# Optimization experiments

Measured on AMD Instinct MI355X. Metric: run time of the kernel, lower is better.

The kernel has to match this reference:

```python
import jax, jax.numpy as jnp
import numpy as np
from jax import lax


def _layernorm(x, g, b, eps=1e-5):
    mu = x.mean(-1, keepdims=True)
    var = ((x - mu) ** 2).mean(-1, keepdims=True)
    return (x - mu) * lax.rsqrt(var + eps) * g + b


def _conv1d(x, w, b):
    # x: (B, T, Cin), w: (K, Cin, Cout) -> (B, T, Cout), SAME padding
    return lax.conv_general_dilated(x, w, (1,), 'SAME',
                                    dimension_numbers=('NWC', 'WIO', 'NWC')) + b


def _gated(x, wf, bf, wg, bg):
    return jax.nn.relu(_conv1d(x, wf, bf)) * jax.nn.sigmoid(_conv1d(x, wg, bg))


def setup_inputs() -> dict:
    key = jax.random.key(0)
    ks = iter(jax.random.split(key, 32))
    B, T, F, H = 32, 1024, 64, 768
    ch = H // 3
    d = {'x': jax.random.normal(next(ks), (B, T, F), jnp.float32)}
    for k in (3, 5, 7):
        d[f'conv{k}_wf'] = jax.random.normal(next(ks), (k, F, ch), jnp.float32) * 0.05
        d[f'conv{k}_bf'] = jnp.zeros((ch,), jnp.float32)
        d[f'conv{k}_wg'] = jax.random.normal(next(ks), (k, F, ch), jnp.float32) * 0.05
        d[f'conv{k}_bg'] = jnp.zeros((ch,), jnp.float32)
    d['conv_ln_g'] = jnp.ones((H,), jnp.float32)
    d['conv_ln_b'] = jnp.zeros((H,), jnp.float32)
    for name in ('gqa_wq', 'gqa_wk', 'gqa_wv', 'gqa_wp'):
        d[name] = jax.random.normal(next(ks), (2, H, H), jnp.float32) * 0.02
    d['gqa_bp'] = jnp.zeros((2, H), jnp.float32)
    d['gqa_ln_g'] = jnp.ones((2, H), jnp.float32)
    d['gqa_ln_b'] = jnp.zeros((2, H), jnp.float32)
    d['proj_w'] = jax.random.normal(next(ks), (2 * H, H), jnp.float32) * 0.02
    d['proj_b'] = jnp.zeros((H,), jnp.float32)
    d['proj_ln_g'] = jnp.ones((H,), jnp.float32)
    d['proj_ln_b'] = jnp.zeros((H,), jnp.float32)
    return d


def _gqa(h, wq, wk, wv, wp, bp, ln_g, ln_b, n_groups=4):
    B, T, H = h.shape
    G, D = n_groups, H // n_groups
    scale = D ** -0.5
    Q = (h @ wq).reshape(B, T, G, D)
    K = (h @ wk).reshape(B, T, G, D)
    V = (h @ wv).reshape(B, T, G, D)
    attn = jax.nn.softmax(jnp.einsum('bqgd,bkgd->bgqk', Q, K) * scale, axis=-1)
    out = jnp.einsum('bgqk,bkgd->bqgd', attn, V).reshape(B, T, H)
    return _layernorm(h + out @ wp + bp, ln_g, ln_b)


def reference(x, conv3_wf, conv3_bf, conv3_wg, conv3_bg,
              conv5_wf, conv5_bf, conv5_wg, conv5_bg,
              conv7_wf, conv7_bf, conv7_wg, conv7_bg,
              conv_ln_g, conv_ln_b,
              gqa_wq, gqa_wk, gqa_wv, gqa_wp, gqa_bp, gqa_ln_g, gqa_ln_b,
              proj_w, proj_b, proj_ln_g, proj_ln_b):
    # Multi-scale gated conv front end (SAME padding -> all branches length T)
    o3 = _gated(x, conv3_wf, conv3_bf, conv3_wg, conv3_bg)
    o5 = _gated(x, conv5_wf, conv5_bf, conv5_wg, conv5_bg)
    o7 = _gated(x, conv7_wf, conv7_bf, conv7_wg, conv7_bg)
    h = _layernorm(jnp.concatenate([o3, o5, o7], axis=-1), conv_ln_g, conv_ln_b)
    # Two GQA blocks
    for i in range(2):
        h = _gqa(h, gqa_wq[i], gqa_wk[i], gqa_wv[i], gqa_wp[i],
                 gqa_bp[i], gqa_ln_g[i], gqa_ln_b[i])
    # mean + population-std pooling over time
    m = h.mean(axis=1)
    s = jnp.sqrt(((h - m[:, None, :]) ** 2).mean(axis=1))
    z = jnp.concatenate([m, s], axis=-1) @ proj_w + proj_b
    return jax.nn.relu(_layernorm(z, proj_ln_g, proj_ln_b))
```

## Files before the change

### kernel.cpp

```cpp
#include <hip/hip_runtime.h>
#include <hip/hip_bf16.h>


constexpr int Bb = 32, Tt = 1024, Ff = 64, Hh = 768, Gg = 4, Dd = 192;
constexpr float EPS = 1e-5f;
constexpr int WKMAX = 448;
constexpr int VTS = 40;

typedef __attribute__((ext_vector_type(8))) short short8;
typedef __attribute__((ext_vector_type(4))) float floatx4;

__device__ __forceinline__ void async_copy16(const void* g, void* l) {
  __builtin_amdgcn_global_load_lds(
      (const __attribute__((address_space(1))) unsigned int*)g,
      (__attribute__((address_space(3))) unsigned int*)l, 16, 0, 0);
}

__device__ __forceinline__ short bf16s(float f) {
  __hip_bfloat16 h = __float2bfloat16(f);
  return *(short*)&h;
}

__device__ __forceinline__ unsigned int pack_bf16(float lo, float hi) {
  return (unsigned int)(unsigned short)bf16s(lo) |
         ((unsigned int)(unsigned short)bf16s(hi) << 16);
}

__device__ __forceinline__ float2 block_reduce2(float a, float b, float* tmp) {
  int lane = threadIdx.x & 63, wid = threadIdx.x >> 6;
#pragma unroll
  for (int off = 32; off > 0; off >>= 1) {
    a += __shfl_down(a, off);
    b += __shfl_down(b, off);
  }
  if (lane == 0) { tmp[wid] = a; tmp[4 + wid] = b; }
  __syncthreads();
  if (threadIdx.x == 0) {
    tmp[0] = tmp[0] + tmp[1] + tmp[2] + tmp[3];
    tmp[4] = tmp[4] + tmp[5] + tmp[6] + tmp[7];
  }
  __syncthreads();
  float2 r; r.x = tmp[0]; r.y = tmp[4];
  return r;
}

__global__ __launch_bounds__(256) void wt_cast_kernel(
    const float* __restrict__ wq, const float* __restrict__ wk,
    const float* __restrict__ wv, const float* __restrict__ wp,
    __hip_bfloat16* __restrict__ wt) {
  const int z = blockIdx.z;
  const int m = z & 3, i = z >> 2;
  const float* src =
      (m == 0 ? wq : m == 1 ? wk : m == 2 ? wv : wp) + (size_t)i * Hh * Hh;
  const float sc = (m == 0) ? 0.0721687836f : 1.f;
  __shared__ float tile[32][33];
  const int n0 = blockIdx.x * 32, k0 = blockIdx.y * 32;
  const int tx = threadIdx.x & 31, ty = threadIdx.x >> 5;
#pragma unroll
  for (int r = 0; r < 4; r++)
    tile[ty + 8 * r][tx] = src[(size_t)(k0 + ty + 8 * r) * Hh + n0 + tx];
  __syncthreads();
#pragma unroll
  for (int r = 0; r < 4; r++)
    wt[((size_t)z * Hh + n0 + ty + 8 * r) * Hh + k0 + tx] =
        __float2bfloat16(tile[tx][ty + 8 * r] * sc);
}

__global__ __launch_bounds__(256) void wcv_cast_kernel(
    const float* __restrict__ wf3, const float* __restrict__ wg3,
    const float* __restrict__ wf5, const float* __restrict__ wg5,
    const float* __restrict__ wf7, const float* __restrict__ wg7,
    __hip_bfloat16* __restrict__ wcv) {
  int idx = blockIdx.x * 256 + threadIdx.x;
  if (idx >= 3 * 512 * WKMAX) return;
  int j = idx / (512 * WKMAX);
  int rem = idx - j * 512 * WKMAX;
  int n = rem / WKMAX, k = rem % WKMAX;
  int Kw = 3 + 2 * j;
  float v = 0.f;
  if (k < Kw * 64) {
    const float* src = (n < 256) ? (j == 0 ? wf3 : j == 1 ? wf5 : wf7)
                                 : (j == 0 ? wg3 : j == 1 ? wg5 : wg7);
    v = src[(size_t)k * 256 + (n & 255)];
  }
  wcv[idx] = __float2bfloat16(v);
}

__global__ __launch_bounds__(256) void x_cast_kernel(
    const float* __restrict__ x, short* __restrict__ x16, int n8) {
  int idx = blockIdx.x * 256 + threadIdx.x;
  if (idx >= n8) return;
  const float4 a = ((const float4*)x)[idx * 2];
  const float4 b = ((const float4*)x)[idx * 2 + 1];
  short8 o;
  o[0] = bf16s(a.x); o[1] = bf16s(a.y); o[2] = bf16s(a.z); o[3] = bf16s(a.w);
  o[4] = bf16s(b.x); o[5] = bf16s(b.y); o[6] = bf16s(b.z); o[7] = bf16s(b.w);
  ((short8*)x16)[idx] = o;
}

__global__ __launch_bounds__(256) void conv_gemm_kernel(
    const short* __restrict__ x16, const short* __restrict__ wcv,
    short* __restrict__ yraw, int b0) {
  __shared__ __align__(16) short Asl[128 * 72];
  __shared__ __align__(16) short Bsl[128 * 72];
  const int t0 = blockIdx.x * 128, n0 = blockIdx.y * 128;
  const int bl = blockIdx.z / 3, j = blockIdx.z % 3;
  const int Kw = 3 + 2 * j, pad = j + 1;
  const int bglob = b0 + bl;
  const short* wb = wcv + (size_t)j * 512 * WKMAX;
  const int tid = threadIdx.x;
  const int lane = tid & 63;
  const int w = tid >> 6, wm = w >> 1, wn = w & 1;
  const int lm = lane & 15, quad = lane >> 4;

  floatx4 acc[4][4];
#pragma unroll
  for (int i = 0; i < 4; i++)
#pragma unroll
    for (int jj = 0; jj < 4; jj++) acc[i][jj] = (floatx4)0.f;

  for (int kk = 0; kk < Kw; kk++) {
    __syncthreads();
#pragma unroll
    for (int it = 0; it < 4; it++) {
      int s = it * 256 + tid;
      int row = s >> 3, c8 = s & 7;
      int t = t0 + row + kk - pad;
      short8 av = (short8)0;
      if (t >= 0 && t < Tt)
        av = *(const short8*)&x16[((size_t)bglob * Tt + t) * Ff + c8 * 8];
      *(short8*)&Asl[row * 72 + c8 * 8] = av;
      short8 bv = *(const short8*)&wb[(size_t)(n0 + row) * WKMAX + kk * 64 +
                                      c8 * 8];
      *(short8*)&Bsl[row * 72 + c8 * 8] = bv;
    }
    __syncthreads();
#pragma unroll
    for (int ks = 0; ks < 2; ks++) {
      short8 a[4], b[4];
#pragma unroll
      for (int i = 0; i < 4; i++)
        a[i] = *(const short8*)&Asl[(wm * 64 + i * 16 + lm) * 72 + ks * 32 +
                                    quad * 8];
#pragma unroll
      for (int jj = 0; jj < 4; jj++)
        b[jj] = *(const short8*)&Bsl[(wn * 64 + jj * 16 + lm) * 72 + ks * 32 +
                                     quad * 8];
#pragma unroll
      for (int i = 0; i < 4; i++)
#pragma unroll
        for (int jj = 0; jj < 4; jj++)
          acc[i][jj] = __builtin_amdgcn_mfma_f32_16x16x32_bf16(a[i], b[jj],
                                                               acc[i][jj],
                                                               0, 0, 0);
    }
  }

  const int rbase = quad * 4;
#pragma unroll
  for (int i = 0; i < 4; i++)
#pragma unroll
    for (int jj = 0; jj < 4; jj++) {
      int mrow = t0 + wm * 64 + i * 16 + rbase;
      int ncol = n0 + wn * 64 + jj * 16 + lm;
#pragma unroll
      for (int r = 0; r < 4; r++)
        yraw[((size_t)bl * Tt + mrow + r) * 1536 + j * 512 + ncol] =
            bf16s(acc[i][jj][r]);
    }
}

__global__ __launch_bounds__(256) void gate_ln_kernel(
    const short* __restrict__ yraw, __hip_bfloat16* __restrict__ h16,
    const float* __restrict__ bf3, const float* __restrict__ bg3,
    const float* __restrict__ bf5, const float* __restrict__ bg5,
    const float* __restrict__ bf7, const float* __restrict__ bg7,
    const float* __restrict__ g, const float* __restrict__ bt) {
  __shared__ float red[8];
  const size_t row = blockIdx.x;
  float v[3], s = 0.f, ss = 0.f;
#pragma unroll
  for (int jj = 0; jj < 3; jj++) {
    int c = threadIdx.x + jj * 256;
    int br = c >> 8, cc = c & 255;
    const float* bfp = br == 0 ? bf3 : br == 1 ? bf5 : bf7;
    const float* bgp = br == 0 ? bg3 : br == 1 ? bg5 : bg7;
    __hip_bfloat16 rf = *(const __hip_bfloat16*)&yraw[row * 1536 + br * 512 + cc];
    __hip_bfloat16 rg =
        *(const __hip_bfloat16*)&yraw[row * 1536 + br * 512 + 256 + cc];
    float f = __bfloat162float(rf) + bfp[cc];
    float gt = __bfloat162float(rg) + bgp[cc];
    float a = f > 0.f ? f : 0.f;
    float t = a * (1.f / (1.f + __expf(-gt)));
    v[jj] = t; s += t; ss += t * t;
  }
  float2 r = block_reduce2(s, ss, red);
  float mu = r.x * (1.f / Hh);
  float var = r.y * (1.f / Hh) - mu * mu;
  float rs = rsqrtf(var + EPS);
#pragma unroll
  for (int jj = 0; jj < 3; jj++) {
    int c = threadIdx.x + jj * 256;
    float o = (v[jj] - mu) * rs * g[c] + bt[c];
    h16[row * Hh + c] = __float2bfloat16(o);
  }
}

__global__ __launch_bounds__(256) void res_ln_kernel(
    __hip_bfloat16* __restrict__ h16, const __hip_bfloat16* __restrict__ y,
    const float* __restrict__ bp, const float* __restrict__ g,
    const float* __restrict__ bt) {
  __shared__ float red[8];
  const size_t row = blockIdx.x;
  float v[3], s = 0.f, ss = 0.f;
#pragma unroll
  for (int jj = 0; jj < 3; jj++) {
    int c = threadIdx.x + jj * 256;
    float t = __bfloat162float(h16[row * Hh + c]) +
              __bfloat162float(y[row * Hh + c]) + bp[c];
    v[jj] = t; s += t; ss += t * t;
  }
  float2 r = block_reduce2(s, ss, red);
  float mu = r.x * (1.f / Hh);
  float var = r.y * (1.f / Hh) - mu * mu;
  float rs = rsqrtf(var + EPS);
#pragma unroll
  for (int jj = 0; jj < 3; jj++) {
    int c = threadIdx.x + jj * 256;
    float o = (v[jj] - mu) * rs * g[c] + bt[c];
    h16[row * Hh + c] = __float2bfloat16(o);
  }
}

__global__ __launch_bounds__(256) void gemm_qkv(
    const short* __restrict__ A, const short* __restrict__ Bt,
    short* __restrict__ q16, short* __restrict__ k16,
    short* __restrict__ vt16) {
  constexpr int K = 768;
  __shared__ __align__(16) short Asl[128 * 32];
  __shared__ __align__(16) short Bsl[128 * 32];
  const int n0 = blockIdx.x * 128, m0 = blockIdx.y * 128;
  const int lane = threadIdx.x & 63;
  const int w = threadIdx.x >> 6, wm = w >> 1, wn = w & 1;
  const int lm = lane & 15, quad = lane >> 4;

  floatx4 acc[4][4];
#pragma unroll
  for (int i = 0; i < 4; i++)
#pragma unroll
    for (int jj = 0; jj < 4; jj++) acc[i][jj] = (floatx4)0.f;

  for (int k0 = 0; k0 < K; k0 += 32) {
    __syncthreads();
#pragma unroll
    for (int half = 0; half < 2; half++) {
      int s = half * 256 + threadIdx.x;
      int m = s >> 2, ks = (s & 3) * 8;
      async_copy16(&A[(size_t)(m0 + m) * K + k0 + ks], &Asl[s * 8]);
      async_copy16(&Bt[(size_t)(n0 + m) * K + k0 + ks], &Bsl[s * 8]);
    }
    __syncthreads();

    short8 a[4], b[4];
#pragma unroll
    for (int i = 0; i < 4; i++)
      a[i] = *(const short8*)&Asl[(wm * 64 + i * 16 + lm) * 32 + quad * 8];
#pragma unroll
    for (int jj = 0; jj < 4; jj++)
      b[jj] = *(const short8*)&Bsl[(wn * 64 + jj * 16 + lm) * 32 + quad * 8];
#pragma unroll
    for (int i = 0; i < 4; i++)
#pragma unroll
      for (int jj = 0; jj < 4; jj++)
        acc[i][jj] = __builtin_amdgcn_mfma_f32_16x16x32_bf16(a[i], b[jj],
                                                             acc[i][jj],
                                                             0, 0, 0);
  }

  const int which = blockIdx.x / 6;
  const int rbase = quad * 4;
#pragma unroll
  for (int i = 0; i < 4; i++)
#pragma unroll
    for (int jj = 0; jj < 4; jj++) {
      int mrow = m0 + wm * 64 + i * 16 + rbase;
      int nl = n0 - which * Hh + wn * 64 + jj * 16 + lm;
      if (which == 0) {
#pragma unroll
        for (int r = 0; r < 4; r++)
          q16[(size_t)(mrow + r) * Hh + nl] = bf16s(acc[i][jj][r]);
      } else if (which == 1) {
#pragma unroll
        for (int r = 0; r < 4; r++)
          k16[(size_t)(mrow + r) * Hh + nl] = bf16s(acc[i][jj][r]);
      } else {
        int bL = mrow >> 10, t = mrow & 1023;
        int g = nl / Dd, d = nl % Dd;
        short4 sv;
        sv.x = bf16s(acc[i][jj][0]); sv.y = bf16s(acc[i][jj][1]);
        sv.z = bf16s(acc[i][jj][2]); sv.w = bf16s(acc[i][jj][3]);
        *(short4*)&vt16[(((size_t)bL * Gg + g) * Dd + d) * Tt + t] = sv;
      }
    }
}

__global__ __launch_bounds__(256) void gemm_proj(
    const short* __restrict__ A, const short* __restrict__ Bt,
    short* __restrict__ C) {
  constexpr int K = 768, N = 768;
  __shared__ __align__(16) short Asl[128 * 32];
  __shared__ __align__(16) short Bsl[128 * 32];
  const int n0 = blockIdx.x * 128, m0 = blockIdx.y * 128;
  const int lane = threadIdx.x & 63;
  const int w = threadIdx.x >> 6, wm = w >> 1, wn = w & 1;
  const int lm = lane & 15, quad = lane >> 4;

  floatx4 acc[4][4];
#pragma unroll
  for (int i = 0; i < 4; i++)
#pragma unroll
    for (int jj = 0; jj < 4; jj++) acc[i][jj] = (floatx4)0.f;

  for (int k0 = 0; k0 < K; k0 += 32) {
    __syncthreads();
#pragma unroll
    for (int half = 0; half < 2; half++) {
      int s = half * 256 + threadIdx.x;
      int m = s >> 2, ks = (s & 3) * 8;
      async_copy16(&A[(size_t)(m0 + m) * K + k0 + ks], &Asl[s * 8]);
      async_copy16(&Bt[(size_t)(n0 + m) * K + k0 + ks], &Bsl[s * 8]);
    }
    __syncthreads();

    short8 a[4], b[4];
#pragma unroll
    for (int i = 0; i < 4; i++)
      a[i] = *(const short8*)&Asl[(wm * 64 + i * 16 + lm) * 32 + quad * 8];
#pragma unroll
    for (int jj = 0; jj < 4; jj++)
      b[jj] = *(const short8*)&Bsl[(wn * 64 + jj * 16 + lm) * 32 + quad * 8];
#pragma unroll
    for (int i = 0; i < 4; i++)
#pragma unroll
      for (int jj = 0; jj < 4; jj++)
        acc[i][jj] = __builtin_amdgcn_mfma_f32_16x16x32_bf16(a[i], b[jj],
                                                             acc[i][jj],
                                                             0, 0, 0);
  }

  const int rbase = quad * 4;
#pragma unroll
  for (int i = 0; i < 4; i++)
#pragma unroll
    for (int jj = 0; jj < 4; jj++) {
      int mrow = m0 + wm * 64 + i * 16 + rbase;
      int ncol = n0 + wn * 64 + jj * 16 + lm;
#pragma unroll
      for (int r = 0; r < 4; r++)
        C[(size_t)(mrow + r) * N + ncol] = bf16s(acc[i][jj][r]);
    }
}

__global__ __launch_bounds__(256, 2) void attn_mfma(
    const short* __restrict__ q16, const short* __restrict__ k16,
    const short* __restrict__ vt16, short* __restrict__ o16) {
  const int b = blockIdx.x;
  const int g = blockIdx.y;
  const int q0 = blockIdx.z * 128;
  const int tid = threadIdx.x;
  const int w = tid >> 6, lane = tid & 63, lm = lane & 15, quad = lane >> 4;

  __shared__ __align__(16) short Ks[32 * 200];
  __shared__ __align__(16) short Vt[192 * VTS];

  short8 qf[2][6];
#pragma unroll
  for (int mt = 0; mt < 2; mt++)
#pragma unroll
    for (int ks = 0; ks < 6; ks++) {
      int tok = b * Tt + q0 + w * 32 + mt * 16 + lm;
      qf[mt][ks] = *(const short8*)&q16[(size_t)tok * Hh + g * Dd + ks * 32 +
                                        quad * 8];
    }

  floatx4 Oa[2][12];
#pragma unroll
  for (int mt = 0; mt < 2; mt++)
#pragma unroll
    for (int n = 0; n < 12; n++) Oa[mt][n] = (floatx4)0.f;
  float mr[2] = {-1e30f, -1e30f}, lr[2] = {0.f, 0.f};

  short8 kvK[3], kvV[3];
#pragma unroll
  for (int it = 0; it < 3; it++) {
    int s = it * 256 + tid;
    int row = s / 24, cs = s - row * 24;
    kvK[it] = *(const short8*)&k16[(size_t)(b * Tt + row) * Hh + g * Dd +
                                   cs * 8];
    int d = s >> 2, c2 = s & 3;
    kvV[it] = *(const short8*)&vt16[(((size_t)b * Gg + g) * Dd + d) * Tt +
                                    c2 * 8];
  }

  for (int kt = 0; kt < Tt; kt += 32) {
    __syncthreads();
#pragma unroll
    for (int it = 0; it < 3; it++) {
      int s = it * 256 + tid;
      int row = s / 24, cs = s - row * 24;
      *(short8*)&Ks[row * 200 + cs * 8] = kvK[it];
      int d = s >> 2, c2 = s & 3;
      *(short8*)&Vt[d * VTS + c2 * 8] = kvV[it];
    }
    __syncthreads();

    if (kt + 32 < Tt) {
#pragma unroll
      for (int it = 0; it < 3; it++) {
        int s = it * 256 + tid;
        int row = s / 24, cs = s - row * 24;
        kvK[it] = *(const short8*)&k16[(size_t)(b * Tt + kt + 32 + row) * Hh +
                                       g * Dd + cs * 8];
        int d = s >> 2, c2 = s & 3;
        kvV[it] = *(const short8*)&vt16[(((size_t)b * Gg + g) * Dd + d) * Tt +
                                        kt + 32 + c2 * 8];
      }
    }

    floatx4 st[2][2];
#pragma unroll
    for (int mt = 0; mt < 2; mt++)
#pragma unroll
      for (int jj = 0; jj < 2; jj++) st[mt][jj] = (floatx4)0.f;
#pragma unroll
    for (int ks = 0; ks < 6; ks++) {
      short8 k0 = *(const short8*)&Ks[lm * 200 + ks * 32 + quad * 8];
      short8 k1 = *(const short8*)&Ks[(16 + lm) * 200 + ks * 32 + quad * 8];
      st[0][0] = __builtin_amdgcn_mfma_f32_16x16x32_bf16(k0, qf[0][ks], st[0][0], 0, 0, 0);
      st[0][1] = __builtin_amdgcn_mfma_f32_16x16x32_bf16(k1, qf[0][ks], st[0][1], 0, 0, 0);
      st[1][0] = __builtin_amdgcn_mfma_f32_16x16x32_bf16(k0, qf[1][ks], st[1][0], 0, 0, 0);
      st[1][1] = __builtin_amdgcn_mfma_f32_16x16x32_bf16(k1, qf[1][ks], st[1][1], 0, 0, 0);
    }

    short8 ptf[2];
#pragma unroll
    for (int mt = 0; mt < 2; mt++) {
      float smax = st[mt][0][0];
#pragma unroll
      for (int r = 1; r < 4; r++) smax = fmaxf(smax, st[mt][0][r]);
#pragma unroll
      for (int r = 0; r < 4; r++) smax = fmaxf(smax, st[mt][1][r]);
      smax = fmaxf(smax, __shfl_xor(smax, 16));
      smax = fmaxf(smax, __shfl_xor(smax, 32));
      float mnew = fmaxf(mr[mt], smax);
      float alpha = __expf(mr[mt] - mnew);
      mr[mt] = mnew;
      float p[2][4];
      float sum = 0.f;
#pragma unroll
      for (int jj = 0; jj < 2; jj++)
#pragma unroll
        for (int r = 0; r < 4; r++) {
          p[jj][r] = __expf(st[mt][jj][r] - mnew);
          sum += p[jj][r];
        }
      sum += __shfl_xor(sum, 16);
      sum += __shfl_xor(sum, 32);
      lr[mt] = lr[mt] * alpha + sum;

      int pk00 = (int)pack_bf16(p[0][0], p[0][1]);
      int pk01 = (int)pack_bf16(p[0][2], p[0][3]);
      int pk10 = (int)pack_bf16(p[1][0], p[1][1]);
      int pk11 = (int)pack_bf16(p[1][2], p[1][3]);
      int srcA = ((quad & 1) << 5) + lm;
      int srcB = srcA + 16;
      int a0 = __shfl(pk00, srcA), a1 = __shfl(pk01, srcA);
      int a2 = __shfl(pk00, srcB), a3 = __shfl(pk01, srcB);
      int b0 = __shfl(pk10, srcA), b1 = __shfl(pk11, srcA);
      int b2 = __shfl(pk10, srcB), b3 = __shfl(pk11, srcB);
      bool hi = quad >= 2;
      union { int u[4]; short8 v; } pu;
      pu.u[0] = hi ? b0 : a0;
      pu.u[1] = hi ? b1 : a1;
      pu.u[2] = hi ? b2 : a2;
      pu.u[3] = hi ? b3 : a3;
      ptf[mt] = pu.v;

#pragma unroll
      for (int n = 0; n < 12; n++)
#pragma unroll
        for (int r = 0; r < 4; r++) Oa[mt][n][r] *= alpha;
    }

#pragma unroll
    for (int n = 0; n < 12; n++) {
      short8 vf = *(const short8*)&Vt[(n * 16 + lm) * VTS + quad * 8];
      Oa[0][n] = __builtin_amdgcn_mfma_f32_16x16x32_bf16(vf, ptf[0], Oa[0][n], 0, 0, 0);
      Oa[1][n] = __builtin_amdgcn_mfma_f32_16x16x32_bf16(vf, ptf[1], Oa[1][n], 0, 0, 0);
    }
  }

#pragma unroll
  for (int mt = 0; mt < 2; mt++) {
    float inv = 1.f / lr[mt];
    int tok = b * Tt + q0 + w * 32 + mt * 16 + lm;
#pragma unroll
    for (int n = 0; n < 12; n++) {
      short4 sv;
      sv.x = bf16s(Oa[mt][n][0] * inv);
      sv.y = bf16s(Oa[mt][n][1] * inv);
      sv.z = bf16s(Oa[mt][n][2] * inv);
      sv.w = bf16s(Oa[mt][n][3] * inv);
      *(short4*)&o16[(size_t)tok * Hh + g * Dd + n * 16 + quad * 4] = sv;
    }
  }
}

__global__ __launch_bounds__(256) void pool_stage1(
    const __hip_bfloat16* __restrict__ h16, float* __restrict__ ppart,
    int b0) {
  int idx = blockIdx.x * 256 + threadIdx.x;
  int seg = blockIdx.y;
  int bl = idx / Hh, c = idx % Hh;
  float s = 0.f, ss = 0.f;
  const __hip_bfloat16* hp = &h16[((size_t)bl * Tt + seg * 128) * Hh + c];
  for (int t = 0; t < 128; t++) {
    float v = __bfloat162float(hp[(size_t)t * Hh]);
    s += v; ss += v * v;
  }
  float* o = &ppart[(((size_t)(b0 + bl) * 8 + seg) * 2) * Hh + c];
  o[0] = s;
  o[Hh] = ss;
}

__global__ __launch_bounds__(256) void pool_stage2(
    const float* __restrict__ ppart, float* __restrict__ pool) {
  int idx = blockIdx.x * 256 + threadIdx.x;
  int b = idx / Hh, c = idx % Hh;
  float s = 0.f, ss = 0.f;
#pragma unroll
  for (int seg = 0; seg < 8; seg++) {
    const float* o = &ppart[(((size_t)b * 8 + seg) * 2) * Hh + c];
    s += o[0]; ss += o[Hh];
  }
  float mu = s * (1.f / Tt);
  float var = ss * (1.f / Tt) - mu * mu;
  pool[(size_t)b * 1536 + c] = mu;
  pool[(size_t)b * 1536 + 768 + c] = sqrtf(fmaxf(var, 0.f));
}

__global__ __launch_bounds__(256) void final_partial(
    const float* __restrict__ pool, const float* __restrict__ pw,
    float* __restrict__ part) {
  const int n = blockIdx.x * 256 + threadIdx.x;
  const int bg = blockIdx.y * 4;
  const int ks = blockIdx.z, k0 = ks * 192;
  __shared__ float ms[4][192];
  for (int e = threadIdx.x; e < 4 * 192; e += 256) {
    int bb = e / 192, kk = e % 192;
    ms[bb][kk] = pool[(size_t)(bg + bb) * 1536 + k0 + kk];
  }
  __syncthreads();
  float a0 = 0.f, a1 = 0.f, a2 = 0.f, a3 = 0.f;
  for (int kk = 0; kk < 192; kk++) {
    float wv = pw[(size_t)(k0 + kk) * Hh + n];
    a0 = fmaf(ms[0][kk], wv, a0);
    a1 = fmaf(ms[1][kk], wv, a1);
    a2 = fmaf(ms[2][kk], wv, a2);
    a3 = fmaf(ms[3][kk], wv, a3);
  }
  part[((size_t)ks * Bb + bg + 0) * Hh + n] = a0;
  part[((size_t)ks * Bb + bg + 1) * Hh + n] = a1;
  part[((size_t)ks * Bb + bg + 2) * Hh + n] = a2;
  part[((size_t)ks * Bb + bg + 3) * Hh + n] = a3;
}

__global__ __launch_bounds__(256) void final_stage2(
    const float* __restrict__ part, const float* __restrict__ pb,
    const float* __restrict__ g, const float* __restrict__ bt,
    float* __restrict__ out) {
  __shared__ float red[8];
  const int b = blockIdx.x;
  float v[3], s = 0.f, ss = 0.f;
#pragma unroll
  for (int jj = 0; jj < 3; jj++) {
    int n = threadIdx.x + jj * 256;
    float a = pb[n];
#pragma unroll
    for (int ks = 0; ks < 8; ks++) a += part[((size_t)ks * Bb + b) * Hh + n];
    v[jj] = a; s += a; ss += a * a;
  }
  float2 r = block_reduce2(s, ss, red);
  float mu = r.x * (1.f / Hh);
  float var = r.y * (1.f / Hh) - mu * mu;
  float rs = rsqrtf(var + EPS);
#pragma unroll
  for (int jj = 0; jj < 3; jj++) {
    int n = threadIdx.x + jj * 256;
    float o = (v[jj] - mu) * rs * g[n] + bt[n];
    out[(size_t)b * Hh + n] = o > 0.f ? o : 0.f;
  }
}

extern "C" void kernel_launch(void* const* d_in, const int* in_sizes, int n_in,
                              void* d_out, int out_size, void* d_ws,
                              size_t ws_size, hipStream_t stream) {
  (void)in_sizes; (void)n_in; (void)out_size;
  const float* x = (const float*)d_in[0];
  const float* cw[3][4];
  for (int j = 0; j < 3; j++)
    for (int p2 = 0; p2 < 4; p2++) cw[j][p2] = (const float*)d_in[1 + j * 4 + p2];
  const float* conv_ln_g = (const float*)d_in[13];
  const float* conv_ln_b = (const float*)d_in[14];
  const float* wq = (const float*)d_in[15];
  const float* wk = (const float*)d_in[16];
  const float* wv = (const float*)d_in[17];
  const float* wp = (const float*)d_in[18];
  const float* bp = (const float*)d_in[19];
  const float* lng = (const float*)d_in[20];
  const float* lnb = (const float*)d_in[21];
  const float* proj_w = (const float*)d_in[22];
  const float* proj_b = (const float*)d_in[23];
  const float* proj_ln_g = (const float*)d_in[24];
  const float* proj_ln_b = (const float*)d_in[25];
  float* out = (float*)d_out;

  const size_t perb = (size_t)Tt * Hh;
  const size_t fixedB = 8ull * Hh * Hh * 2 + 3ull * 512 * WKMAX * 2 +
                        (size_t)Bb * Tt * Ff * 2 + (size_t)Bb * 2 * Hh * 4 +
                        (size_t)Bb * 8 * 2 * Hh * 4 + 8ull * Bb * Hh * 4;
  int chunk = Bb;
  while (chunk > 1 && 8ull * perb * chunk + fixedB > ws_size) chunk >>= 1;

  const size_t crow = perb * (size_t)chunk;
  char* p = (char*)d_ws;
  __hip_bfloat16* h16 = (__hip_bfloat16*)p;  p += crow * 2;
  short* q16 = (short*)p;            p += crow * 2;
  short* k16 = (short*)p;            p += crow * 2;
  short* v16t = (short*)p;           p += crow * 2;
  short* yraw16 = q16;
  short* y16 = k16;
  __hip_bfloat16* wt = (__hip_bfloat16*)p;   p += 8ull * Hh * Hh * 2;
  __hip_bfloat16* wcv = (__hip_bfloat16*)p;  p += 3ull * 512 * WKMAX * 2;
  short* x16 = (short*)p;            p += (size_t)Bb * Tt * Ff * 2;
  float* pool = (float*)p;           p += (size_t)Bb * 2 * Hh * 4;
  float* ppart = (float*)p;          p += (size_t)Bb * 8 * 2 * Hh * 4;
  float* fpart = (float*)p;

  wt_cast_kernel<<<dim3(24, 24, 8), 256, 0, stream>>>(wq, wk, wv, wp, wt);
  wcv_cast_kernel<<<(3 * 512 * WKMAX + 255) / 256, 256, 0, stream>>>(
      cw[0][0], cw[0][2], cw[1][0], cw[1][2], cw[2][0], cw[2][2], wcv);
  x_cast_kernel<<<(Bb * Tt * Ff / 8 + 255) / 256, 256, 0, stream>>>(
      x, x16, Bb * Tt * Ff / 8);

  const short* wts = (const short*)wt;

  for (int b0 = 0; b0 < Bb; b0 += chunk) {
    const int M = chunk * Tt;

    conv_gemm_kernel<<<dim3(Tt / 128, 4, chunk * 3), 256, 0, stream>>>(
        x16, (const short*)wcv, yraw16, b0);
    gate_ln_kernel<<<M, 256, 0, stream>>>(
        yraw16, h16, cw[0][1], cw[0][3], cw[1][1], cw[1][3], cw[2][1],
        cw[2][3], conv_ln_g, conv_ln_b);

    for (int i = 0; i < 2; i++) {
      const short* wqkv = wts + (size_t)(i * 4) * Hh * Hh;
      const short* wtp = wts + (size_t)(i * 4 + 3) * Hh * Hh;
      gemm_qkv<<<dim3(18, M / 128), 256, 0, stream>>>((const short*)h16, wqkv,
                                                      q16, k16, v16t);
      attn_mfma<<<dim3(chunk, Gg, Tt / 128), 256, 0, stream>>>(q16, k16, v16t,
                                                               q16);
      gemm_proj<<<dim3(6, M / 128), 256, 0, stream>>>(q16, wtp, y16);
      res_ln_kernel<<<M, 256, 0, stream>>>(h16, (const __hip_bfloat16*)y16,
                                           bp + (size_t)i * Hh,
                                           lng + (size_t)i * Hh,
                                           lnb + (size_t)i * Hh);
    }

    pool_stage1<<<dim3((chunk * Hh) / 256, 8), 256, 0, stream>>>(h16, ppart,
                                                                 b0);
  }

  pool_stage2<<<(Bb * Hh) / 256, 256, 0, stream>>>(ppart, pool);
  final_partial<<<dim3(3, 8, 8), 256, 0, stream>>>(pool, proj_w, fpart);
  final_stage2<<<Bb, 256, 0, stream>>>(fpart, proj_b, proj_ln_g, proj_ln_b,
                                       out);
}
```

Measured before the change: 1.066 ms.

## Double-buffer K/V tiles in attention and fold row-sum into MFMA

The attention kernel now keeps two LDS buffers for K and V^T tiles, cutting the per-iteration barrier count from two to one and prefetching two tiles ahead in registers. It also appends a ones-row to the V^T tile so a 13th MFMA column accumulates the softmax denominator, replacing the per-tile shuffle reductions for the row sum. The cost is roughly double the LDS footprint, which may reduce occupancy, one extra MFMA per tile, and a denominator summed from bf16-rounded probabilities.

```diff
diff --git a/kernel.cpp b/kernel.cpp
--- a/kernel.cpp
+++ b/kernel.cpp
@@ -370,8 +370,16 @@
   const int tid = threadIdx.x;
   const int w = tid >> 6, lane = tid & 63, lm = lane & 15, quad = lane >> 4;
 
-  __shared__ __align__(16) short Ks[32 * 200];
-  __shared__ __align__(16) short Vt[192 * VTS];
+  __shared__ __align__(16) short Ks[2][32 * 200];
+  __shared__ __align__(16) short Vt[2][208 * VTS];
+
+  for (int e = tid; e < 2 * 16 * VTS; e += 256) {
+    int buf = e / (16 * VTS);
+    int r = e - buf * (16 * VTS);
+    int row = r / VTS, c = r - row * VTS;
+    Vt[buf][(192 + row) * VTS + c] =
+        (row == 0 && c < 32) ? (short)0x3F80 : (short)0;
+  }
 
   short8 qf[2][6];
 #pragma unroll
@@ -383,49 +391,62 @@
                                         quad * 8];
     }
 
-  floatx4 Oa[2][12];
+  floatx4 Oa[2][13];
 #pragma unroll
   for (int mt = 0; mt < 2; mt++)
 #pragma unroll
-    for (int n = 0; n < 12; n++) Oa[mt][n] = (floatx4)0.f;
-  float mr[2] = {-1e30f, -1e30f}, lr[2] = {0.f, 0.f};
-
-  short8 kvK[3], kvV[3];
+    for (int n = 0; n < 13; n++) Oa[mt][n] = (floatx4)0.f;
+  float mr[2] = {-1e30f, -1e30f};
+
+  int krow[3], kcs[3], vrow[3], vcs[3];
+  const short* kgp[3];
+  const short* vgp[3];
 #pragma unroll
   for (int it = 0; it < 3; it++) {
     int s = it * 256 + tid;
-    int row = s / 24, cs = s - row * 24;
-    kvK[it] = *(const short8*)&k16[(size_t)(b * Tt + row) * Hh + g * Dd +
-                                   cs * 8];
-    int d = s >> 2, c2 = s & 3;
-    kvV[it] = *(const short8*)&vt16[(((size_t)b * Gg + g) * Dd + d) * Tt +
-                                    c2 * 8];
-  }
-
-  for (int kt = 0; kt < Tt; kt += 32) {
-    __syncthreads();
-#pragma unroll
-    for (int it = 0; it < 3; it++) {
-      int s = it * 256 + tid;
-      int row = s / 24, cs = s - row * 24;
-      *(short8*)&Ks[row * 200 + cs * 8] = kvK[it];
-      int d = s >> 2, c2 = s & 3;
-      *(short8*)&Vt[d * VTS + c2 * 8] = kvV[it];
-    }
-    __syncthreads();
-
-    if (kt + 32 < Tt) {
+    krow[it] = s / 24; kcs[it] = s - krow[it] * 24;
+    vrow[it] = s >> 2; vcs[it] = s & 3;
+    kgp[it] = &k16[(size_t)(b * Tt + krow[it]) * Hh + g * Dd + kcs[it] * 8];
+    vgp[it] = &vt16[(((size_t)b * Gg + g) * Dd + vrow[it]) * Tt + vcs[it] * 8];
+  }
+
+  short8 kvK[3], kvV[3];
+#pragma unroll
+  for (int it = 0; it < 3; it++) {
+    kvK[it] = *(const short8*)kgp[it];
+    kvV[it] = *(const short8*)vgp[it];
+  }
+#pragma unroll
+  for (int it = 0; it < 3; it++) {
+    *(short8*)&Ks[0][krow[it] * 200 + kcs[it] * 8] = kvK[it];
+    *(short8*)&Vt[0][vrow[it] * VTS + vcs[it] * 8] = kvV[it];
+  }
+#pragma unroll
+  for (int it = 0; it < 3; it++) {
+    kvK[it] = *(const short8*)(kgp[it] + (size_t)32 * Hh);
+    kvV[it] = *(const short8*)(vgp[it] + 32);
+  }
+  __syncthreads();
+
+  for (int i = 0; i < 32; i++) {
+    const int ib = i & 1;
+    if (i + 1 < 32) {
+      const int wb2 = ib ^ 1;
 #pragma unroll
       for (int it = 0; it < 3; it++) {
-        int s = it * 256 + tid;
-        int row = s / 24, cs = s - row * 24;
-        kvK[it] = *(const short8*)&k16[(size_t)(b * Tt + kt + 32 + row) * Hh +
-                                       g * Dd + cs * 8];
-        int d = s >> 2, c2 = s & 3;
-        kvV[it] = *(const short8*)&vt16[(((size_t)b * Gg + g) * Dd + d) * Tt +
-                                        kt + 32 + c2 * 8];
+        *(short8*)&Ks[wb2][krow[it] * 200 + kcs[it] * 8] = kvK[it];
+        *(short8*)&Vt[wb2][vrow[it] * VTS + vcs[it] * 8] = kvV[it];
       }
     }
+    if (i + 2 < 32) {
+      const size_t ko = (size_t)(i + 2) * 32 * Hh;
+      const int vo = (i + 2) * 32;
+#pragma unroll
+      for (int it = 0; it < 3; it++) {
+        kvK[it] = *(const short8*)(kgp[it] + ko);
+        kvV[it] = *(const short8*)(vgp[it] + vo);
+      }
+    }
 
     floatx4 st[2][2];
 #pragma unroll
@@ -434,8 +455,8 @@
       for (int jj = 0; jj < 2; jj++) st[mt][jj] = (floatx4)0.f;
 #pragma unroll
     for (int ks = 0; ks < 6; ks++) {
-      short8 k0 = *(const short8*)&Ks[lm * 200 + ks * 32 + quad * 8];
-      short8 k1 = *(const short8*)&Ks[(16 + lm) * 200 + ks * 32 + quad * 8];
+      short8 k0 = *(const short8*)&Ks[ib][lm * 200 + ks * 32 + quad * 8];
+      short8 k1 = *(const short8*)&Ks[ib][(16 + lm) * 200 + ks * 32 + quad * 8];
       st[0][0] = __builtin_amdgcn_mfma_f32_16x16x32_bf16(k0, qf[0][ks], st[0][0], 0, 0, 0);
       st[0][1] = __builtin_amdgcn_mfma_f32_16x16x32_bf16(k1, qf[0][ks], st[0][1], 0, 0, 0);
       st[1][0] = __builtin_amdgcn_mfma_f32_16x16x32_bf16(k0, qf[1][ks], st[1][0], 0, 0, 0);
@@ -456,17 +477,10 @@
       float alpha = __expf(mr[mt] - mnew);
       mr[mt] = mnew;
       float p[2][4];
-      float sum = 0.f;
 #pragma unroll
       for (int jj = 0; jj < 2; jj++)
 #pragma unroll
-        for (int r = 0; r < 4; r++) {
-          p[jj][r] = __expf(st[mt][jj][r] - mnew);
-          sum += p[jj][r];
-        }
-      sum += __shfl_xor(sum, 16);
-      sum += __shfl_xor(sum, 32);
-      lr[mt] = lr[mt] * alpha + sum;
+        for (int r = 0; r < 4; r++) p[jj][r] = __expf(st[mt][jj][r] - mnew);
 
       int pk00 = (int)pack_bf16(p[0][0], p[0][1]);
       int pk01 = (int)pack_bf16(p[0][2], p[0][3]);
@@ -487,22 +501,24 @@
       ptf[mt] = pu.v;
 
 #pragma unroll
-      for (int n = 0; n < 12; n++)
+      for (int n = 0; n < 13; n++)
 #pragma unroll
         for (int r = 0; r < 4; r++) Oa[mt][n][r] *= alpha;
     }
 
 #pragma unroll
-    for (int n = 0; n < 12; n++) {
-      short8 vf = *(const short8*)&Vt[(n * 16 + lm) * VTS + quad * 8];
+    for (int n = 0; n < 13; n++) {
+      short8 vf = *(const short8*)&Vt[ib][(n * 16 + lm) * VTS + quad * 8];
       Oa[0][n] = __builtin_amdgcn_mfma_f32_16x16x32_bf16(vf, ptf[0], Oa[0][n], 0, 0, 0);
       Oa[1][n] = __builtin_amdgcn_mfma_f32_16x16x32_bf16(vf, ptf[1], Oa[1][n], 0, 0, 0);
     }
+    __syncthreads();
   }
 
 #pragma unroll
   for (int mt = 0; mt < 2; mt++) {
-    float inv = 1.f / lr[mt];
+    float lval = __shfl(Oa[mt][12][0], lm);
+    float inv = 1.f / lval;
     int tok = b * Tt + q0 + w * 32 + mt * 16 + lm;
 #pragma unroll
     for (int n = 0; n < 12; n++) {
```

Result: no change. 1.048 ms (-1.7%).

## Restructure attention: 64-query blocks, async double-buffered V, MFMA row-sum

Applied to the files above, without the earlier changes.

The attention kernel now gives each wave 16 query rows instead of 32, halving accumulator registers so occupancy can rise to 4 blocks per CU. The grid is flattened with batch-group varying fastest so neighbouring blocks share K/V. V tiles are loaded with global_load_lds async copies into a double buffer, and K is still staged through registers. The softmax denominator is computed by a 13th MFMA against a ones-padded V row rather than shuffle reductions; this adds MFMA work and LDS use, and QK work per block is amortised over fewer queries.

```diff
diff --git a/kernel.cpp b/kernel.cpp
--- a/kernel.cpp
+++ b/kernel.cpp
@@ -5,7 +5,6 @@
 constexpr int Bb = 32, Tt = 1024, Ff = 64, Hh = 768, Gg = 4, Dd = 192;
 constexpr float EPS = 1e-5f;
 constexpr int WKMAX = 448;
-constexpr int VTS = 40;
 
 typedef __attribute__((ext_vector_type(8))) short short8;
 typedef __attribute__((ext_vector_type(4))) float floatx4;
@@ -361,158 +360,145 @@
     }
 }
 
-__global__ __launch_bounds__(256, 2) void attn_mfma(
+__global__ __launch_bounds__(256, 4) void attn_mfma(
     const short* __restrict__ q16, const short* __restrict__ k16,
-    const short* __restrict__ vt16, short* __restrict__ o16) {
-  const int b = blockIdx.x;
-  const int g = blockIdx.y;
-  const int q0 = blockIdx.z * 128;
+    const short* __restrict__ vt16, short* __restrict__ o16, int chunk4) {
+  const int bg = blockIdx.x % chunk4;
+  const int qb = blockIdx.x / chunk4;
+  const int b = bg >> 2, g = bg & 3;
+  const int q0 = qb * 64;
   const int tid = threadIdx.x;
   const int w = tid >> 6, lane = tid & 63, lm = lane & 15, quad = lane >> 4;
 
   __shared__ __align__(16) short Ks[32 * 200];
-  __shared__ __align__(16) short Vt[192 * VTS];
-
-  short8 qf[2][6];
-#pragma unroll
-  for (int mt = 0; mt < 2; mt++)
-#pragma unroll
-    for (int ks = 0; ks < 6; ks++) {
-      int tok = b * Tt + q0 + w * 32 + mt * 16 + lm;
-      qf[mt][ks] = *(const short8*)&q16[(size_t)tok * Hh + g * Dd + ks * 32 +
-                                        quad * 8];
-    }
-
-  floatx4 Oa[2][12];
-#pragma unroll
-  for (int mt = 0; mt < 2; mt++)
-#pragma unroll
-    for (int n = 0; n < 12; n++) Oa[mt][n] = (floatx4)0.f;
-  float mr[2] = {-1e30f, -1e30f}, lr[2] = {0.f, 0.f};
-
-  short8 kvK[3], kvV[3];
+  __shared__ __align__(16) short Vt[2][208 * 32];
+  constexpr int VBUF = 208 * 32;
+
+  for (int e = tid; e < 2 * 16 * 32; e += 256) {
+    int buf = e >> 9;
+    int r = e & 511;
+    Vt[buf][192 * 32 + r] = (r < 32) ? (short)0x3F80 : (short)0;
+  }
+
+  short8 qf[6];
+  {
+    int tok = b * Tt + q0 + w * 16 + lm;
+#pragma unroll
+    for (int ks = 0; ks < 6; ks++)
+      qf[ks] = *(const short8*)&q16[(size_t)tok * Hh + g * Dd + ks * 32 +
+                                    quad * 8];
+  }
+
+  floatx4 Oa[13];
+#pragma unroll
+  for (int n = 0; n < 13; n++) Oa[n] = (floatx4)0.f;
+  float mr = -1e30f;
+
+  int krow[3], kcs[3];
+  const short* kgp[3];
+  const short* vgp[3];
+  short* vld[3];
 #pragma unroll
   for (int it = 0; it < 3; it++) {
     int s = it * 256 + tid;
-    int row = s / 24, cs = s - row * 24;
-    kvK[it] = *(const short8*)&k16[(size_t)(b * Tt + row) * Hh + g * Dd +
-                                   cs * 8];
-    int d = s >> 2, c2 = s & 3;
-    kvV[it] = *(const short8*)&vt16[(((size_t)b * Gg + g) * Dd + d) * Tt +
-                                    c2 * 8];
-  }
-
-  for (int kt = 0; kt < Tt; kt += 32) {
-    __syncthreads();
-#pragma unroll
-    for (int it = 0; it < 3; it++) {
-      int s = it * 256 + tid;
-      int row = s / 24, cs = s - row * 24;
-      *(short8*)&Ks[row * 200 + cs * 8] = kvK[it];
-      int d = s >> 2, c2 = s & 3;
-      *(short8*)&Vt[d * VTS + c2 * 8] = kvV[it];
-    }
-    __syncthreads();
-
-    if (kt + 32 < Tt) {
-#pragma unroll
-      for (int it = 0; it < 3; it++) {
-        int s = it * 256 + tid;
-        int row = s / 24, cs = s - row * 24;
-        kvK[it] = *(const short8*)&k16[(size_t)(b * Tt + kt + 32 + row) * Hh +
-                                       g * Dd + cs * 8];
-        int d = s >> 2, c2 = s & 3;
-        kvV[it] = *(const short8*)&vt16[(((size_t)b * Gg + g) * Dd + d) * Tt +
-                                        kt + 32 + c2 * 8];
-      }
-    }
-
-    floatx4 st[2][2];
-#pragma unroll
-    for (int mt = 0; mt < 2; mt++)
-#pragma unroll
-      for (int jj = 0; jj < 2; jj++) st[mt][jj] = (floatx4)0.f;
+    krow[it] = s / 24; kcs[it] = s - krow[it] * 24;
+    kgp[it] = &k16[(size_t)(b * Tt + krow[it]) * Hh + g * Dd + kcs[it] * 8];
+    int d = s >> 2, cs = s & 3;
+    vgp[it] = &vt16[(((size_t)b * Gg + g) * Dd + d) * Tt + cs * 8];
+    vld[it] = (short*)&Vt[0][0] + (size_t)s * 8;
+  }
+
+  short8 kvK[3];
+#pragma unroll
+  for (int it = 0; it < 3; it++) kvK[it] = *(const short8*)kgp[it];
+#pragma unroll
+  for (int it = 0; it < 3; it++) async_copy16(vgp[it], vld[it]);
+
+  for (int i = 0; i < 32; i++) {
+    const int ib = i & 1;
+    __syncthreads();
+#pragma unroll
+    for (int it = 0; it < 3; it++)
+      *(short8*)&Ks[krow[it] * 200 + kcs[it] * 8] = kvK[it];
+    __syncthreads();
+
+    if (i + 1 < 32) {
+      const int vo = (i + 1) * 32;
+#pragma unroll
+      for (int it = 0; it < 3; it++)
+        async_copy16(vgp[it] + vo, vld[it] + (ib ^ 1) * VBUF);
+      const size_t ko = (size_t)(i + 1) * 32 * Hh;
+#pragma unroll
+      for (int it = 0; it < 3; it++) kvK[it] = *(const short8*)(kgp[it] + ko);
+    }
+
+    floatx4 st[2];
+    st[0] = (floatx4)0.f; st[1] = (floatx4)0.f;
 #pragma unroll
     for (int ks = 0; ks < 6; ks++) {
       short8 k0 = *(const short8*)&Ks[lm * 200 + ks * 32 + quad * 8];
       short8 k1 = *(const short8*)&Ks[(16 + lm) * 200 + ks * 32 + quad * 8];
-      st[0][0] = __builtin_amdgcn_mfma_f32_16x16x32_bf16(k0, qf[0][ks], st[0][0], 0, 0, 0);
-      st[0][1] = __builtin_amdgcn_mfma_f32_16x16x32_bf16(k1, qf[0][ks], st[0][1], 0, 0, 0);
-      st[1][0] = __builtin_amdgcn_mfma_f32_16x16x32_bf16(k0, qf[1][ks], st[1][0], 0, 0, 0);
-      st[1][1] = __builtin_amdgcn_mfma_f32_16x16x32_bf16(k1, qf[1][ks], st[1][1], 0, 0, 0);
-    }
-
-    short8 ptf[2];
-#pragma unroll
-    for (int mt = 0; mt < 2; mt++) {
-      float smax = st[mt][0][0];
-#pragma unroll
-      for (int r = 1; r < 4; r++) smax = fmaxf(smax, st[mt][0][r]);
-#pragma unroll
-      for (int r = 0; r < 4; r++) smax = fmaxf(smax, st[mt][1][r]);
-      smax = fmaxf(smax, __shfl_xor(smax, 16));
-      smax = fmaxf(smax, __shfl_xor(smax, 32));
-      float mnew = fmaxf(mr[mt], smax);
-      float alpha = __expf(mr[mt] - mnew);
-      mr[mt] = mnew;
-      float p[2][4];
-      float sum = 0.f;
-#pragma unroll
-      for (int jj = 0; jj < 2; jj++)
-#pragma unroll
-        for (int r = 0; r < 4; r++) {
-          p[jj][r] = __expf(st[mt][jj][r] - mnew);
-          sum += p[jj][r];
-        }
-      sum += __shfl_xor(sum, 16);
-      sum += __shfl_xor(sum, 32);
-      lr[mt] = lr[mt] * alpha + sum;
-
-      int pk00 = (int)pack_bf16(p[0][0], p[0][1]);
-      int pk01 = (int)pack_bf16(p[0][2], p[0][3]);
-      int pk10 = (int)pack_bf16(p[1][0], p[1][1]);
-      int pk11 = (int)pack_bf16(p[1][2], p[1][3]);
-      int srcA = ((quad & 1) << 5) + lm;
-      int srcB = srcA + 16;
-      int a0 = __shfl(pk00, srcA), a1 = __shfl(pk01, srcA);
-      int a2 = __shfl(pk00, srcB), a3 = __shfl(pk01, srcB);
-      int b0 = __shfl(pk10, srcA), b1 = __shfl(pk11, srcA);
-      int b2 = __shfl(pk10, srcB), b3 = __shfl(pk11, srcB);
-      bool hi = quad >= 2;
-      union { int u[4]; short8 v; } pu;
-      pu.u[0] = hi ? b0 : a0;
-      pu.u[1] = hi ? b1 : a1;
-      pu.u[2] = hi ? b2 : a2;
-      pu.u[3] = hi ? b3 : a3;
-      ptf[mt] = pu.v;
-
-#pragma unroll
-      for (int n = 0; n < 12; n++)
-#pragma unroll
-        for (int r = 0; r < 4; r++) Oa[mt][n][r] *= alpha;
-    }
-
-#pragma unroll
-    for (int n = 0; n < 12; n++) {
-      short8 vf = *(const short8*)&Vt[(n * 16 + lm) * VTS + quad * 8];
-      Oa[0][n] = __builtin_amdgcn_mfma_f32_16x16x32_bf16(vf, ptf[0], Oa[0][n], 0, 0, 0);
-      Oa[1][n] = __builtin_amdgcn_mfma_f32_16x16x32_bf16(vf, ptf[1], Oa[1][n], 0, 0, 0);
-    }
-  }
-
-#pragma unroll
-  for (int mt = 0; mt < 2; mt++) {
-    float inv = 1.f / lr[mt];
-    int tok = b * Tt + q0 + w * 32 + mt * 16 + lm;
-#pragma unroll
-    for (int n = 0; n < 12; n++) {
-      short4 sv;
-      sv.x = bf16s(Oa[mt][n][0] * inv);
-      sv.y = bf16s(Oa[mt][n][1] * inv);
-      sv.z = bf16s(Oa[mt][n][2] * inv);
-      sv.w = bf16s(Oa[mt][n][3] * inv);
-      *(short4*)&o16[(size_t)tok * Hh + g * Dd + n * 16 + quad * 4] = sv;
-    }
+      st[0] = __builtin_amdgcn_mfma_f32_16x16x32_bf16(k0, qf[ks], st[0], 0, 0, 0);
+      st[1] = __builtin_amdgcn_mfma_f32_16x16x32_bf16(k1, qf[ks], st[1], 0, 0, 0);
+    }
+
+    float smax = st[0][0];
+#pragma unroll
+    for (int r = 1; r < 4; r++) smax = fmaxf(smax, st[0][r]);
+#pragma unroll
+    for (int r = 0; r < 4; r++) smax = fmaxf(smax, st[1][r]);
+    smax = fmaxf(smax, __shfl_xor(smax, 16));
+    smax = fmaxf(smax, __shfl_xor(smax, 32));
+    float mnew = fmaxf(mr, smax);
+    float alpha = __expf(mr - mnew);
+    mr = mnew;
+    float p[2][4];
+#pragma unroll
+    for (int jj = 0; jj < 2; jj++)
+#pragma unroll
+      for (int r = 0; r < 4; r++) p[jj][r] = __expf(st[jj][r] - mnew);
+
+    int pk00 = (int)pack_bf16(p[0][0], p[0][1]);
+    int pk01 = (int)pack_bf16(p[0][2], p[0][3]);
+    int pk10 = (int)pack_bf16(p[1][0], p[1][1]);
+    int pk11 = (int)pack_bf16(p[1][2], p[1][3]);
+    int srcA = ((quad & 1) << 5) + lm;
+    int srcB = srcA + 16;
+    int a0 = __shfl(pk00, srcA), a1 = __shfl(pk01, srcA);
+    int a2 = __shfl(pk00, srcB), a3 = __shfl(pk01, srcB);
+    int b0 = __shfl(pk10, srcA), b1 = __shfl(pk11, srcA);
+    int b2 = __shfl(pk10, srcB), b3 = __shfl(pk11, srcB);
+    bool hi = quad >= 2;
+    union { int u[4]; short8 v; } pu;
+    pu.u[0] = hi ? b0 : a0;
+    pu.u[1] = hi ? b1 : a1;
+    pu.u[2] = hi ? b2 : a2;
+    pu.u[3] = hi ? b3 : a3;
+    short8 ptf = pu.v;
+
+#pragma unroll
+    for (int n = 0; n < 13; n++)
+#pragma unroll
+      for (int r = 0; r < 4; r++) Oa[n][r] *= alpha;
+
+#pragma unroll
+    for (int n = 0; n < 13; n++) {
+      short8 vf = *(const short8*)&Vt[ib][(n * 16 + lm) * 32 + quad * 8];
+      Oa[n] = __builtin_amdgcn_mfma_f32_16x16x32_bf16(vf, ptf, Oa[n], 0, 0, 0);
+    }
+  }
+
+  float lval = __shfl(Oa[12][0], lm);
+  float inv = 1.f / lval;
+  int tok = b * Tt + q0 + w * 16 + lm;
+#pragma unroll
+  for (int n = 0; n < 12; n++) {
+    short4 sv;
+    sv.x = bf16s(Oa[n][0] * inv);
+    sv.y = bf16s(Oa[n][1] * inv);
+    sv.z = bf16s(Oa[n][2] * inv);
+    sv.w = bf16s(Oa[n][3] * inv);
+    *(short4*)&o16[(size_t)tok * Hh + g * Dd + n * 16 + quad * 4] = sv;
   }
 }
 
@@ -669,8 +655,8 @@
       const short* wtp = wts + (size_t)(i * 4 + 3) * Hh * Hh;
       gemm_qkv<<<dim3(18, M / 128), 256, 0, stream>>>((const short*)h16, wqkv,
                                                       q16, k16, v16t);
-      attn_mfma<<<dim3(chunk, Gg, Tt / 128), 256, 0, stream>>>(q16, k16, v16t,
-                                                               q16);
+      attn_mfma<<<dim3(chunk * Gg * (Tt / 64)), 256, 0, stream>>>(
+          q16, k16, v16t, q16, chunk * Gg);
       gemm_proj<<<dim3(6, M / 128), 256, 0, stream>>>(q16, wtp, y16);
       res_ln_kernel<<<M, 256, 0, stream>>>(h16, (const __hip_bfloat16*)y16,
                                            bp + (size_t)i * Hh,
```

New measurement: 1.118 ms. 1.05x slower.
